# Kernel tuning notes

Hardware: AMD Instinct MI355X
Metric: run time of the kernel (lower is better)

## Reference

```python
import jax, jax.numpy as jnp
import numpy as np


def setup_inputs() -> dict:
    key = jax.random.key(0)
    ks = jax.random.split(key, 7)
    N, D_IN, D_HID, D_OUT, DEPTH = 1048576, 64, 128, 64, 4
    s_in = 1.0 / np.sqrt(D_IN)
    s_h = 1.0 / np.sqrt(D_HID)
    return {
        "x": jax.random.normal(ks[0], (N, D_IN), dtype=jnp.float32),
        "w_in": jax.random.normal(ks[1], (D_HID, D_IN), dtype=jnp.float32) * s_in,
        "b_in": jax.random.normal(ks[2], (D_HID,), dtype=jnp.float32) * s_in,
        "w_hid": jax.random.normal(ks[3], ((DEPTH - 1) * D_HID, D_HID), dtype=jnp.float32) * s_h,
        "b_hid": jax.random.normal(ks[4], (DEPTH - 1, D_HID), dtype=jnp.float32) * s_h,
        "w_out": jax.random.normal(ks[5], (D_OUT, D_HID), dtype=jnp.float32) * s_h,
        "b_out": jax.random.normal(ks[6], (D_OUT,), dtype=jnp.float32) * s_h,
    }


def reference(x, w_in, b_in, w_hid, b_hid, w_out, b_out):
    # Fully-fused MLP: in-layer + (depth-1) hidden layers + out-layer.
    # nn.Linear convention: y = x @ W.T + b. ReLU after input and hidden layers,
    # no activation on the output layer (tiny-cuda-nn convention).
    d_hidden = w_in.shape[0]
    n_hidden = b_hid.shape[0]  # depth - 1
    w_hid_l = w_hid.reshape(n_hidden, d_hidden, d_hidden)  # [L, d_hid, d_hid]
    h = jax.nn.relu(jnp.einsum("nd,hd->nh", x, w_in) + b_in)  # [N, d_hid]
    for l in range(n_hidden):  # small fixed depth loop
        h = jax.nn.relu(jnp.einsum("nd,hd->nh", h, w_hid_l[l]) + b_hid[l])
    out = jnp.einsum("nh,oh->no", h, w_out) + b_out  # [N, d_out]
    return out
```

## Files before the change

### kernel.cpp

```cpp
#include <hip/hip_runtime.h>
#include <stdint.h>


#define D_IN   64
#define D_HID  128
#define D_OUT  64
#define N_HID  3
#define NT     4
#define WAVES  8
#define BLOCK  (WAVES * 64)
#define GRID   256
#define ITERS  8
#define ROWS_PER_WAVE (NT * 16)
#define ROWS_PER_BLOCK (WAVES * ROWS_PER_WAVE)

#define L0_OFF   0
#define H_OFF    8192
#define H_STRIDE 16384
#define OUT_OFF  57344
#define W_ELEMS  65536
#define LDS_BYTES (W_ELEMS * 2 + 576 * 4)

typedef __attribute__((ext_vector_type(8))) short  short8;
typedef __attribute__((ext_vector_type(4))) float  floatx4;

union U4 { short8 s8; unsigned int u[4]; };

__device__ __forceinline__ unsigned int bfround(unsigned int u) {
  return u + 0x7fffu + ((u >> 16) & 1u);
}
__device__ __forceinline__ unsigned int cvt_pk_bf16(float lo, float hi) {
  unsigned int r;
  asm("v_cvt_pk_bf16_f32 %0, %1, %2" : "=v"(r) : "v"(lo), "v"(hi));
  return r;
}
__device__ __forceinline__ floatx4 mfma16(short8 a, short8 b, floatx4 c) {
  return __builtin_amdgcn_mfma_f32_16x16x32_bf16(a, b, c, 0, 0, 0);
}
__device__ __forceinline__ short8 ldsfrag(const unsigned short* p) {
  short8 v;
  __builtin_memcpy(&v, __builtin_assume_aligned(p, 16), 16);
  return v;
}
__device__ __forceinline__ floatx4 ldsbias(const float* p) {
  floatx4 v;
  __builtin_memcpy(&v, __builtin_assume_aligned(p, 16), 16);
  return v;
}

#define W_IN_ELEMS  (D_HID * D_IN)
#define W_HID_ELEMS (N_HID * D_HID * D_HID)
#define W_OUT_ELEMS (D_OUT * D_HID)

__device__ __forceinline__ int kperm(int kp) {
  return 32 * (kp >> 5) + 16 * ((kp >> 2) & 1) + 4 * ((kp >> 3) & 3) + (kp & 3);
}

__global__ void wconvert_kernel(const float* __restrict__ w_in,
                                const float* __restrict__ w_hid,
                                const float* __restrict__ w_out,
                                unsigned short* __restrict__ wbf) {
  const int i = blockIdx.x * 256 + threadIdx.x;
  float v;
  if (i < H_OFF) {
    const int mt = i >> 10;
    const int r  = i & 1023;
    const int s  = r >> 9;
    const int l  = (r >> 3) & 63;
    const int j  = r & 7;
    const int c = l & 15, q = l >> 4;
    v = w_in[(mt * 16 + c) * D_IN + s * 32 + q * 8 + j];
  } else if (i < OUT_OFF) {
    const int ii = i - H_OFF;
    const int lh = ii >> 14;
    const int r0 = ii & 16383;
    const int mt = r0 >> 11;
    const int r  = r0 & 2047;
    const int s  = r >> 9;
    const int l  = (r >> 3) & 63;
    const int j  = r & 7;
    const int c = l & 15, q = l >> 4;
    v = w_hid[lh * (D_HID * D_HID) + (mt * 16 + c) * D_HID + kperm(s * 32 + q * 8 + j)];
  } else {
    const int ii = i - OUT_OFF;
    const int mt = ii >> 11;
    const int r  = ii & 2047;
    const int s  = r >> 9;
    const int l  = (r >> 3) & 63;
    const int j  = r & 7;
    const int c = l & 15, q = l >> 4;
    v = w_out[(mt * 16 + c) * D_HID + kperm(s * 32 + q * 8 + j)];
  }
  wbf[i] = (unsigned short)(bfround(__float_as_uint(v)) >> 16);
}

__device__ __forceinline__ void hidden_layer(const U4 (&bin)[NT][4], U4 (&bout)[NT][4],
                                             const unsigned short* __restrict__ fb,
                                             const float* __restrict__ blds,
                                             int lh, int q) {
  const unsigned short* wl = fb + H_OFF + lh * H_STRIDE;
  const float* bl = blds + 128 + lh * 128;
#pragma unroll
  for (int mt = 0; mt < 8; ++mt) {
    short8 a0 = ldsfrag(wl + (mt * 4 + 0) * 512);
    short8 a1 = ldsfrag(wl + (mt * 4 + 1) * 512);
    short8 a2 = ldsfrag(wl + (mt * 4 + 2) * 512);
    short8 a3 = ldsfrag(wl + (mt * 4 + 3) * 512);
    floatx4 bias = ldsbias(bl + mt * 16 + q * 4);
#pragma unroll
    for (int nt = 0; nt < NT; ++nt) {
      floatx4 acc = bias;
      acc = mfma16(a0, bin[nt][0].s8, acc);
      acc = mfma16(a1, bin[nt][1].s8, acc);
      acc = mfma16(a2, bin[nt][2].s8, acc);
      acc = mfma16(a3, bin[nt][3].s8, acc);
      bout[nt][mt >> 1].u[2 * (mt & 1) + 0] =
          cvt_pk_bf16(fmaxf(acc[0], 0.f), fmaxf(acc[1], 0.f));
      bout[nt][mt >> 1].u[2 * (mt & 1) + 1] =
          cvt_pk_bf16(fmaxf(acc[2], 0.f), fmaxf(acc[3], 0.f));
    }
  }
}

__global__ __launch_bounds__(BLOCK, 2) void mlp_kernel(
    const float* __restrict__ x,
    const unsigned short* __restrict__ wbf,
    const float* __restrict__ b_in,
    const float* __restrict__ b_hid,
    const float* __restrict__ b_out,
    float* __restrict__ out) {
  extern __shared__ unsigned short wlds[];
  const int tid  = threadIdx.x;
  const int wv   = tid >> 6;
  const int lane = tid & 63;
  const int q    = lane >> 4;
  const int c    = lane & 15;

  {
    uint4* dst = (uint4*)wlds;
    const uint4* src = (const uint4*)wbf;
#pragma unroll
    for (int i = 0; i < 16; ++i) dst[tid + i * BLOCK] = src[tid + i * BLOCK];
    float* bl = (float*)(wlds + W_ELEMS);
    if (tid < 128) bl[tid] = b_in[tid];
    if (tid < 384) bl[128 + tid] = b_hid[tid];
    if (tid < 64)  bl[512 + tid] = b_out[tid];
  }
  __syncthreads();

  const unsigned short* fb = wlds + lane * 8;
  const float* blds = (const float*)(wlds + W_ELEMS);

  U4 ba[NT][4], bb[NT][4];
  floatx4 px[16];

  {
    const int rb = blockIdx.x * ROWS_PER_BLOCK + wv * ROWS_PER_WAVE;
#pragma unroll
    for (int nt = 0; nt < NT; ++nt) {
      const float* xr = x + (rb + nt * 16 + c) * D_IN + q * 8;
      px[nt * 4 + 0] = *(const floatx4*)(xr);
      px[nt * 4 + 1] = *(const floatx4*)(xr + 4);
      px[nt * 4 + 2] = *(const floatx4*)(xr + 32);
      px[nt * 4 + 3] = *(const floatx4*)(xr + 36);
    }
  }

  for (int it = 0; it < ITERS; ++it) {
    const int rb = (it * GRID + blockIdx.x) * ROWS_PER_BLOCK + wv * ROWS_PER_WAVE;

#pragma unroll
    for (int nt = 0; nt < NT; ++nt) {
      U4 b0, b1;
      b0.u[0] = cvt_pk_bf16(px[nt * 4 + 0][0], px[nt * 4 + 0][1]);
      b0.u[1] = cvt_pk_bf16(px[nt * 4 + 0][2], px[nt * 4 + 0][3]);
      b0.u[2] = cvt_pk_bf16(px[nt * 4 + 1][0], px[nt * 4 + 1][1]);
      b0.u[3] = cvt_pk_bf16(px[nt * 4 + 1][2], px[nt * 4 + 1][3]);
      b1.u[0] = cvt_pk_bf16(px[nt * 4 + 2][0], px[nt * 4 + 2][1]);
      b1.u[1] = cvt_pk_bf16(px[nt * 4 + 2][2], px[nt * 4 + 2][3]);
      b1.u[2] = cvt_pk_bf16(px[nt * 4 + 3][0], px[nt * 4 + 3][1]);
      b1.u[3] = cvt_pk_bf16(px[nt * 4 + 3][2], px[nt * 4 + 3][3]);
#pragma unroll
      for (int mt = 0; mt < 8; ++mt) {
        short8 a0 = ldsfrag(fb + L0_OFF + (mt * 2 + 0) * 512);
        short8 a1 = ldsfrag(fb + L0_OFF + (mt * 2 + 1) * 512);
        floatx4 acc = ldsbias(blds + mt * 16 + q * 4);
        acc = mfma16(a0, b0.s8, acc);
        acc = mfma16(a1, b1.s8, acc);
        bb[nt][mt >> 1].u[2 * (mt & 1) + 0] =
            cvt_pk_bf16(fmaxf(acc[0], 0.f), fmaxf(acc[1], 0.f));
        bb[nt][mt >> 1].u[2 * (mt & 1) + 1] =
            cvt_pk_bf16(fmaxf(acc[2], 0.f), fmaxf(acc[3], 0.f));
      }
    }

    hidden_layer(bb, ba, fb, blds, 0, q);
    hidden_layer(ba, bb, fb, blds, 1, q);
    hidden_layer(bb, ba, fb, blds, 2, q);

    if (it + 1 < ITERS) {
      const int nrb = ((it + 1) * GRID + blockIdx.x) * ROWS_PER_BLOCK + wv * ROWS_PER_WAVE;
#pragma unroll
      for (int nt = 0; nt < NT; ++nt) {
        const float* xr = x + (nrb + nt * 16 + c) * D_IN + q * 8;
        px[nt * 4 + 0] = *(const floatx4*)(xr);
        px[nt * 4 + 1] = *(const floatx4*)(xr + 4);
        px[nt * 4 + 2] = *(const floatx4*)(xr + 32);
        px[nt * 4 + 3] = *(const floatx4*)(xr + 36);
      }
    }

#pragma unroll
    for (int mt = 0; mt < 4; ++mt) {
      short8 a0 = ldsfrag(fb + OUT_OFF + (mt * 4 + 0) * 512);
      short8 a1 = ldsfrag(fb + OUT_OFF + (mt * 4 + 1) * 512);
      short8 a2 = ldsfrag(fb + OUT_OFF + (mt * 4 + 2) * 512);
      short8 a3 = ldsfrag(fb + OUT_OFF + (mt * 4 + 3) * 512);
      floatx4 bias = ldsbias(blds + 512 + mt * 16 + q * 4);
#pragma unroll
      for (int nt = 0; nt < NT; ++nt) {
        floatx4 acc = bias;
        acc = mfma16(a0, ba[nt][0].s8, acc);
        acc = mfma16(a1, ba[nt][1].s8, acc);
        acc = mfma16(a2, ba[nt][2].s8, acc);
        acc = mfma16(a3, ba[nt][3].s8, acc);
        *(floatx4*)(out + (rb + nt * 16 + c) * D_OUT + mt * 16 + q * 4) = acc;
      }
    }
  }
}

extern "C" void kernel_launch(void* const* d_in, const int* in_sizes, int n_in,
                              void* d_out, int out_size, void* d_ws, size_t ws_size,
                              hipStream_t stream) {
  const float* x     = (const float*)d_in[0];
  const float* w_in  = (const float*)d_in[1];
  const float* b_in  = (const float*)d_in[2];
  const float* w_hid = (const float*)d_in[3];
  const float* b_hid = (const float*)d_in[4];
  const float* w_out = (const float*)d_in[5];
  const float* b_out = (const float*)d_in[6];
  float* out = (float*)d_out;
  unsigned short* wbf = (unsigned short*)d_ws;

  wconvert_kernel<<<W_ELEMS / 256, 256, 0, stream>>>(w_in, w_hid, w_out, wbf);

  (void)hipFuncSetAttribute((const void*)mlp_kernel,
                            hipFuncAttributeMaxDynamicSharedMemorySize, LDS_BYTES);

  mlp_kernel<<<GRID, BLOCK, LDS_BYTES, stream>>>(x, wbf, b_in, b_hid, b_out, out);
}
```

Measured before the change: 481.2 us.

## Double block waves, split input prefetch, reorder layer-0 loops for A-fragment reuse

Doubles waves per block to 16 and halves per-block iterations, so the same 256-block grid covers all rows with more waves resident per CU. The input prefetch is split into two halves issued at different points in the loop. Layer 0 now loads each weight fragment once and applies it to all four row tiles instead of reloading it per tile. The outer loop is kept rolled. Launch bounds are raised to 4, which tightens the register budget and risks spills. Weight LDS staging is adjusted to the larger block.

```diff
diff --git a/kernel.cpp b/kernel.cpp
--- a/kernel.cpp
+++ b/kernel.cpp
@@ -7,10 +7,10 @@
 #define D_OUT  64
 #define N_HID  3
 #define NT     4
-#define WAVES  8
+#define WAVES  16
 #define BLOCK  (WAVES * 64)
 #define GRID   256
-#define ITERS  8
+#define ITERS  4
 #define ROWS_PER_WAVE (NT * 16)
 #define ROWS_PER_BLOCK (WAVES * ROWS_PER_WAVE)
 
@@ -122,7 +122,7 @@
   }
 }
 
-__global__ __launch_bounds__(BLOCK, 2) void mlp_kernel(
+__global__ __launch_bounds__(BLOCK, 4) void mlp_kernel(
     const float* __restrict__ x,
     const unsigned short* __restrict__ wbf,
     const float* __restrict__ b_in,
@@ -140,7 +140,7 @@
     uint4* dst = (uint4*)wlds;
     const uint4* src = (const uint4*)wbf;
 #pragma unroll
-    for (int i = 0; i < 16; ++i) dst[tid + i * BLOCK] = src[tid + i * BLOCK];
+    for (int i = 0; i < 8; ++i) dst[tid + i * BLOCK] = src[tid + i * BLOCK];
     float* bl = (float*)(wlds + W_ELEMS);
     if (tid < 128) bl[tid] = b_in[tid];
     if (tid < 384) bl[128 + tid] = b_hid[tid];
@@ -152,41 +152,62 @@
   const float* blds = (const float*)(wlds + W_ELEMS);
 
   U4 ba[NT][4], bb[NT][4];
-  floatx4 px[16];
+  floatx4 p1[8], p2[8];
 
   {
     const int rb = blockIdx.x * ROWS_PER_BLOCK + wv * ROWS_PER_WAVE;
 #pragma unroll
-    for (int nt = 0; nt < NT; ++nt) {
-      const float* xr = x + (rb + nt * 16 + c) * D_IN + q * 8;
-      px[nt * 4 + 0] = *(const floatx4*)(xr);
-      px[nt * 4 + 1] = *(const floatx4*)(xr + 4);
-      px[nt * 4 + 2] = *(const floatx4*)(xr + 32);
-      px[nt * 4 + 3] = *(const floatx4*)(xr + 36);
-    }
-  }
-
+    for (int h = 0; h < 2; ++h) {
+      const float* xr = x + (rb + h * 16 + c) * D_IN + q * 8;
+      p1[h * 4 + 0] = *(const floatx4*)(xr);
+      p1[h * 4 + 1] = *(const floatx4*)(xr + 4);
+      p1[h * 4 + 2] = *(const floatx4*)(xr + 32);
+      p1[h * 4 + 3] = *(const floatx4*)(xr + 36);
+    }
+#pragma unroll
+    for (int h = 0; h < 2; ++h) {
+      const float* xr = x + (rb + (h + 2) * 16 + c) * D_IN + q * 8;
+      p2[h * 4 + 0] = *(const floatx4*)(xr);
+      p2[h * 4 + 1] = *(const floatx4*)(xr + 4);
+      p2[h * 4 + 2] = *(const floatx4*)(xr + 32);
+      p2[h * 4 + 3] = *(const floatx4*)(xr + 36);
+    }
+  }
+
+#pragma unroll 1
   for (int it = 0; it < ITERS; ++it) {
     const int rb = (it * GRID + blockIdx.x) * ROWS_PER_BLOCK + wv * ROWS_PER_WAVE;
 
-#pragma unroll
-    for (int nt = 0; nt < NT; ++nt) {
-      U4 b0, b1;
-      b0.u[0] = cvt_pk_bf16(px[nt * 4 + 0][0], px[nt * 4 + 0][1]);
-      b0.u[1] = cvt_pk_bf16(px[nt * 4 + 0][2], px[nt * 4 + 0][3]);
-      b0.u[2] = cvt_pk_bf16(px[nt * 4 + 1][0], px[nt * 4 + 1][1]);
-      b0.u[3] = cvt_pk_bf16(px[nt * 4 + 1][2], px[nt * 4 + 1][3]);
-      b1.u[0] = cvt_pk_bf16(px[nt * 4 + 2][0], px[nt * 4 + 2][1]);
-      b1.u[1] = cvt_pk_bf16(px[nt * 4 + 2][2], px[nt * 4 + 2][3]);
-      b1.u[2] = cvt_pk_bf16(px[nt * 4 + 3][0], px[nt * 4 + 3][1]);
-      b1.u[3] = cvt_pk_bf16(px[nt * 4 + 3][2], px[nt * 4 + 3][3]);
-#pragma unroll
-      for (int mt = 0; mt < 8; ++mt) {
-        short8 a0 = ldsfrag(fb + L0_OFF + (mt * 2 + 0) * 512);
-        short8 a1 = ldsfrag(fb + L0_OFF + (mt * 2 + 1) * 512);
-        floatx4 acc = ldsbias(blds + mt * 16 + q * 4);
-        acc = mfma16(a0, b0.s8, acc);
-        acc = mfma16(a1, b1.s8, acc);
+    U4 bx[NT][2];
+#pragma unroll
+    for (int h = 0; h < 2; ++h) {
+      bx[h][0].u[0] = cvt_pk_bf16(p1[h * 4 + 0][0], p1[h * 4 + 0][1]);
+      bx[h][0].u[1] = cvt_pk_bf16(p1[h * 4 + 0][2], p1[h * 4 + 0][3]);
+      bx[h][0].u[2] = cvt_pk_bf16(p1[h * 4 + 1][0], p1[h * 4 + 1][1]);
+      bx[h][0].u[3] = cvt_pk_bf16(p1[h * 4 + 1][2], p1[h * 4 + 1][3]);
+      bx[h][1].u[0] = cvt_pk_bf16(p1[h * 4 + 2][0], p1[h * 4 + 2][1]);
+      bx[h][1].u[1] = cvt_pk_bf16(p1[h * 4 + 2][2], p1[h * 4 + 2][3]);
+      bx[h][1].u[2] = cvt_pk_bf16(p1[h * 4 + 3][0], p1[h * 4 + 3][1]);
+      bx[h][1].u[3] = cvt_pk_bf16(p1[h * 4 + 3][2], p1[h * 4 + 3][3]);
+      bx[h + 2][0].u[0] = cvt_pk_bf16(p2[h * 4 + 0][0], p2[h * 4 + 0][1]);
+      bx[h + 2][0].u[1] = cvt_pk_bf16(p2[h * 4 + 0][2], p2[h * 4 + 0][3]);
+      bx[h + 2][0].u[2] = cvt_pk_bf16(p2[h * 4 + 1][0], p2[h * 4 + 1][1]);
+      bx[h + 2][0].u[3] = cvt_pk_bf16(p2[h * 4 + 1][2], p2[h * 4 + 1][3]);
+      bx[h + 2][1].u[0] = cvt_pk_bf16(p2[h * 4 + 2][0], p2[h * 4 + 2][1]);
+      bx[h + 2][1].u[1] = cvt_pk_bf16(p2[h * 4 + 2][2], p2[h * 4 + 2][3]);
+      bx[h + 2][1].u[2] = cvt_pk_bf16(p2[h * 4 + 3][0], p2[h * 4 + 3][1]);
+      bx[h + 2][1].u[3] = cvt_pk_bf16(p2[h * 4 + 3][2], p2[h * 4 + 3][3]);
+    }
+#pragma unroll
+    for (int mt = 0; mt < 8; ++mt) {
+      short8 a0 = ldsfrag(fb + L0_OFF + (mt * 2 + 0) * 512);
+      short8 a1 = ldsfrag(fb + L0_OFF + (mt * 2 + 1) * 512);
+      floatx4 bias = ldsbias(blds + mt * 16 + q * 4);
+#pragma unroll
+      for (int nt = 0; nt < NT; ++nt) {
+        floatx4 acc = bias;
+        acc = mfma16(a0, bx[nt][0].s8, acc);
+        acc = mfma16(a1, bx[nt][1].s8, acc);
         bb[nt][mt >> 1].u[2 * (mt & 1) + 0] =
             cvt_pk_bf16(fmaxf(acc[0], 0.f), fmaxf(acc[1], 0.f));
         bb[nt][mt >> 1].u[2 * (mt & 1) + 1] =
@@ -201,12 +222,12 @@
     if (it + 1 < ITERS) {
       const int nrb = ((it + 1) * GRID + blockIdx.x) * ROWS_PER_BLOCK + wv * ROWS_PER_WAVE;
 #pragma unroll
-      for (int nt = 0; nt < NT; ++nt) {
-        const float* xr = x + (nrb + nt * 16 + c) * D_IN + q * 8;
-        px[nt * 4 + 0] = *(const floatx4*)(xr);
-        px[nt * 4 + 1] = *(const floatx4*)(xr + 4);
-        px[nt * 4 + 2] = *(const floatx4*)(xr + 32);
-        px[nt * 4 + 3] = *(const floatx4*)(xr + 36);
+      for (int h = 0; h < 2; ++h) {
+        const float* xr = x + (nrb + h * 16 + c) * D_IN + q * 8;
+        p1[h * 4 + 0] = *(const floatx4*)(xr);
+        p1[h * 4 + 1] = *(const floatx4*)(xr + 4);
+        p1[h * 4 + 2] = *(const floatx4*)(xr + 32);
+        p1[h * 4 + 3] = *(const floatx4*)(xr + 36);
       }
     }
 
@@ -225,6 +246,18 @@
         acc = mfma16(a2, ba[nt][2].s8, acc);
         acc = mfma16(a3, ba[nt][3].s8, acc);
         *(floatx4*)(out + (rb + nt * 16 + c) * D_OUT + mt * 16 + q * 4) = acc;
+      }
+    }
+
+    if (it + 1 < ITERS) {
+      const int nrb = ((it + 1) * GRID + blockIdx.x) * ROWS_PER_BLOCK + wv * ROWS_PER_WAVE;
+#pragma unroll
+      for (int h = 0; h < 2; ++h) {
+        const float* xr = x + (nrb + (h + 2) * 16 + c) * D_IN + q * 8;
+        p2[h * 4 + 0] = *(const floatx4*)(xr);
+        p2[h * 4 + 1] = *(const floatx4*)(xr + 4);
+        p2[h * 4 + 2] = *(const floatx4*)(xr + 32);
+        p2[h * 4 + 3] = *(const floatx4*)(xr + 36);
       }
     }
   }
```

Result: slower. 707.8 us (+47.1%).

## Use 12-wave blocks with a contiguous per-block row range and strided chunk scheduling

Applied to the files above, without the earlier changes.

Raises the block size from 8 to 12 waves and pins occupancy at 3 waves per EU, so one 4096-row contiguous block range is split into 64-row chunks handed out round-robin to the waves. The first layer is reordered to reuse each weight fragment across all four row tiles, which cuts repeated LDS fragment loads. The weight copy loop is adjusted for the new block size. The change aims to better hide latency, but 64 chunks do not divide evenly across 12 waves, so some waves do an extra chunk and the block finishes unevenly.

```diff
diff --git a/kernel.cpp b/kernel.cpp
--- a/kernel.cpp
+++ b/kernel.cpp
@@ -7,12 +7,11 @@
 #define D_OUT  64
 #define N_HID  3
 #define NT     4
-#define WAVES  8
+#define WAVES  12
 #define BLOCK  (WAVES * 64)
 #define GRID   256
-#define ITERS  8
-#define ROWS_PER_WAVE (NT * 16)
-#define ROWS_PER_BLOCK (WAVES * ROWS_PER_WAVE)
+#define CHUNKS 64
+#define ROWS_PER_BLOCK 4096
 
 #define L0_OFF   0
 #define H_OFF    8192
@@ -122,7 +121,9 @@
   }
 }
 
-__global__ __launch_bounds__(BLOCK, 2) void mlp_kernel(
+__global__ __launch_bounds__(BLOCK)
+__attribute__((amdgpu_waves_per_eu(3, 3)))
+void mlp_kernel(
     const float* __restrict__ x,
     const unsigned short* __restrict__ wbf,
     const float* __restrict__ b_in,
@@ -140,7 +141,10 @@
     uint4* dst = (uint4*)wlds;
     const uint4* src = (const uint4*)wbf;
 #pragma unroll
-    for (int i = 0; i < 16; ++i) dst[tid + i * BLOCK] = src[tid + i * BLOCK];
+    for (int i = 0; i < 11; ++i) {
+      const int idx = tid + i * BLOCK;
+      if (idx < W_ELEMS / 8) dst[idx] = src[idx];
+    }
     float* bl = (float*)(wlds + W_ELEMS);
     if (tid < 128) bl[tid] = b_in[tid];
     if (tid < 384) bl[128 + tid] = b_hid[tid];
@@ -154,8 +158,10 @@
   U4 ba[NT][4], bb[NT][4];
   floatx4 px[16];
 
+  const int blockrow = blockIdx.x * ROWS_PER_BLOCK;
+
   {
-    const int rb = blockIdx.x * ROWS_PER_BLOCK + wv * ROWS_PER_WAVE;
+    const int rb = blockrow + wv * 64;
 #pragma unroll
     for (int nt = 0; nt < NT; ++nt) {
       const float* xr = x + (rb + nt * 16 + c) * D_IN + q * 8;
@@ -166,27 +172,32 @@
     }
   }
 
-  for (int it = 0; it < ITERS; ++it) {
-    const int rb = (it * GRID + blockIdx.x) * ROWS_PER_BLOCK + wv * ROWS_PER_WAVE;
-
+#pragma unroll 1
+  for (int ck = wv; ck < CHUNKS; ck += WAVES) {
+    const int rb = blockrow + ck * 64;
+
+    U4 bx[NT][2];
 #pragma unroll
     for (int nt = 0; nt < NT; ++nt) {
-      U4 b0, b1;
-      b0.u[0] = cvt_pk_bf16(px[nt * 4 + 0][0], px[nt * 4 + 0][1]);
-      b0.u[1] = cvt_pk_bf16(px[nt * 4 + 0][2], px[nt * 4 + 0][3]);
-      b0.u[2] = cvt_pk_bf16(px[nt * 4 + 1][0], px[nt * 4 + 1][1]);
-      b0.u[3] = cvt_pk_bf16(px[nt * 4 + 1][2], px[nt * 4 + 1][3]);
-      b1.u[0] = cvt_pk_bf16(px[nt * 4 + 2][0], px[nt * 4 + 2][1]);
-      b1.u[1] = cvt_pk_bf16(px[nt * 4 + 2][2], px[nt * 4 + 2][3]);
-      b1.u[2] = cvt_pk_bf16(px[nt * 4 + 3][0], px[nt * 4 + 3][1]);
-      b1.u[3] = cvt_pk_bf16(px[nt * 4 + 3][2], px[nt * 4 + 3][3]);
-#pragma unroll
-      for (int mt = 0; mt < 8; ++mt) {
-        short8 a0 = ldsfrag(fb + L0_OFF + (mt * 2 + 0) * 512);
-        short8 a1 = ldsfrag(fb + L0_OFF + (mt * 2 + 1) * 512);
-        floatx4 acc = ldsbias(blds + mt * 16 + q * 4);
-        acc = mfma16(a0, b0.s8, acc);
-        acc = mfma16(a1, b1.s8, acc);
+      bx[nt][0].u[0] = cvt_pk_bf16(px[nt * 4 + 0][0], px[nt * 4 + 0][1]);
+      bx[nt][0].u[1] = cvt_pk_bf16(px[nt * 4 + 0][2], px[nt * 4 + 0][3]);
+      bx[nt][0].u[2] = cvt_pk_bf16(px[nt * 4 + 1][0], px[nt * 4 + 1][1]);
+      bx[nt][0].u[3] = cvt_pk_bf16(px[nt * 4 + 1][2], px[nt * 4 + 1][3]);
+      bx[nt][1].u[0] = cvt_pk_bf16(px[nt * 4 + 2][0], px[nt * 4 + 2][1]);
+      bx[nt][1].u[1] = cvt_pk_bf16(px[nt * 4 + 2][2], px[nt * 4 + 2][3]);
+      bx[nt][1].u[2] = cvt_pk_bf16(px[nt * 4 + 3][0], px[nt * 4 + 3][1]);
+      bx[nt][1].u[3] = cvt_pk_bf16(px[nt * 4 + 3][2], px[nt * 4 + 3][3]);
+    }
+#pragma unroll
+    for (int mt = 0; mt < 8; ++mt) {
+      short8 a0 = ldsfrag(fb + L0_OFF + (mt * 2 + 0) * 512);
+      short8 a1 = ldsfrag(fb + L0_OFF + (mt * 2 + 1) * 512);
+      floatx4 bias = ldsbias(blds + mt * 16 + q * 4);
+#pragma unroll
+      for (int nt = 0; nt < NT; ++nt) {
+        floatx4 acc = bias;
+        acc = mfma16(a0, bx[nt][0].s8, acc);
+        acc = mfma16(a1, bx[nt][1].s8, acc);
         bb[nt][mt >> 1].u[2 * (mt & 1) + 0] =
             cvt_pk_bf16(fmaxf(acc[0], 0.f), fmaxf(acc[1], 0.f));
         bb[nt][mt >> 1].u[2 * (mt & 1) + 1] =
@@ -198,8 +209,8 @@
     hidden_layer(ba, bb, fb, blds, 1, q);
     hidden_layer(bb, ba, fb, blds, 2, q);
 
-    if (it + 1 < ITERS) {
-      const int nrb = ((it + 1) * GRID + blockIdx.x) * ROWS_PER_BLOCK + wv * ROWS_PER_WAVE;
+    if (ck + WAVES < CHUNKS) {
+      const int nrb = blockrow + (ck + WAVES) * 64;
 #pragma unroll
       for (int nt = 0; nt < NT; ++nt) {
         const float* xr = x + (nrb + nt * 16 + c) * D_IN + q * 8;
```

Measured after the change: 566.9 us. +17.8%, slower.
